# Kernel tuning notes

Hardware: AMD Instinct MI355X
Metric: run time of the kernel (lower is better)

The kernel has to match this reference:

```python
import jax, jax.numpy as jnp
import numpy as np

# hyper_params (mode='test')
PRE_NMS = 1000
POST_NMS = 300
IOU_TH = 0.7
VARIANCES = np.array([0.1, 0.1, 0.2, 0.2], dtype=np.float32)
FM = 64            # feature map height/width
ANCHOR_COUNT = 9   # 3 scales x 3 ratios


def _make_anchors():
    """Normalized [y1,x1,y2,x2] anchors on a FM x FM grid, 9 per cell."""
    scales = np.array([0.1, 0.2, 0.4], np.float32)
    ratios = np.array([0.5, 1.0, 2.0], np.float32)
    ws = (scales[:, None] * np.sqrt(ratios)[None, :]).reshape(-1)  # (9,)
    hs = (scales[:, None] / np.sqrt(ratios)[None, :]).reshape(-1)  # (9,)
    ctr = (np.arange(FM, dtype=np.float32) + 0.5) / FM
    cy, cx = np.meshgrid(ctr, ctr, indexing='ij')                  # (FM,FM)
    cy = cy[..., None]; cx = cx[..., None]                         # (FM,FM,1)
    anchors = np.stack([cy - 0.5 * hs, cx - 0.5 * ws,
                        cy + 0.5 * hs, cx + 0.5 * ws], axis=-1)    # (FM,FM,9,4)
    return jnp.asarray(anchors.reshape(-1, 4))                     # (36864,4)


def setup_inputs() -> dict:
    key = jax.random.key(0)
    k1, k2 = jax.random.split(key)
    B = 16
    rpn_bbox_deltas = jax.random.normal(k1, (B, FM, FM, ANCHOR_COUNT * 4), dtype=jnp.float32)
    rpn_labels = jax.random.uniform(k2, (B, FM, FM, ANCHOR_COUNT), dtype=jnp.float32)
    return {"rpn_bbox_deltas": rpn_bbox_deltas,
            "rpn_labels": rpn_labels,
            "anchors": _make_anchors()}


def _nms_single(boxes):
    """Greedy NMS on score-sorted boxes (N,4) -> (POST_NMS,4), zero-padded."""
    N = boxes.shape[0]
    y1, x1, y2, x2 = boxes[:, 0], boxes[:, 1], boxes[:, 2], boxes[:, 3]
    area = (y2 - y1) * (x2 - x1)                                   # (N,)
    iy1 = jnp.maximum(y1[:, None], y1[None, :])
    ix1 = jnp.maximum(x1[:, None], x1[None, :])
    iy2 = jnp.minimum(y2[:, None], y2[None, :])
    ix2 = jnp.minimum(x2[:, None], x2[None, :])
    inter = jnp.maximum(iy2 - iy1, 0.0) * jnp.maximum(ix2 - ix1, 0.0)
    iou = inter / jnp.maximum(area[:, None] + area[None, :] - inter, 1e-9)  # (N,N)
    idx = jnp.arange(N)

    def body(i, keep):
        # if box i survives, suppress later boxes with high overlap
        suppress = keep[i] & (iou[i] > IOU_TH) & (idx > i)
        return keep & ~suppress

    keep = jax.lax.fori_loop(0, N, body, jnp.ones((N,), dtype=bool))
    # stable sort: kept boxes first, original (score-descending) order preserved
    order = jnp.argsort(jnp.where(keep, 0, 1))[:POST_NMS]
    sel = boxes[order]
    valid = keep[order]
    # combined_non_max_suppression clips output boxes to [0,1] and zero-pads
    return jnp.where(valid[:, None], jnp.clip(sel, 0.0, 1.0), 0.0)


def reference(rpn_bbox_deltas, rpn_labels, anchors):
    B = rpn_bbox_deltas.shape[0]
    N = anchors.shape[0]
    deltas = rpn_bbox_deltas.reshape(B, N, 4) * jnp.asarray(VARIANCES)
    labels = rpn_labels.reshape(B, N)

    # decode deltas against anchors
    anc_h = anchors[:, 2] - anchors[:, 0]
    anc_w = anchors[:, 3] - anchors[:, 1]
    anc_cy = anchors[:, 0] + 0.5 * anc_h
    anc_cx = anchors[:, 1] + 0.5 * anc_w
    h = jnp.exp(deltas[..., 2]) * anc_h
    w = jnp.exp(deltas[..., 3]) * anc_w
    cy = deltas[..., 0] * anc_h + anc_cy
    cx = deltas[..., 1] * anc_w + anc_cx
    boxes = jnp.stack([cy - 0.5 * h, cx - 0.5 * w,
                       cy + 0.5 * h, cx + 0.5 * w], axis=-1)       # (B,N,4)

    # top-k by objectness score (descending, so NMS input is pre-sorted)
    _, pre_idx = jax.lax.top_k(labels, PRE_NMS)                    # (B,PRE_NMS)
    pre_boxes = jnp.take_along_axis(boxes, pre_idx[..., None], axis=1)  # (B,PRE_NMS,4)

    roi_bboxes = jax.vmap(_nms_single)(pre_boxes)                  # (B,POST_NMS,4)
    return jax.lax.stop_gradient(roi_bboxes)
```

## Files before the change

kernel.cpp:

```cpp
#include <hip/hip_runtime.h>
#include <stdint.h>

#pragma clang fp contract(off)

#define N_ANCH 36864
#define PRE_NMS 1000
#define POST_NMS 300
#define SEL_CAP 1024
#define NWAVE 16

#define SLICES 16
#define K1_NT 256
#define SLICE_KEYS 2304
#define KEYS_PT 9
#define SLICE_TOP 128
#define COMPACT_CAP 192
#define MERGE_CAP 2048

#define NCOPY 8
#define HSTR 257

#define M_WSTRIDE 1024
#define M_WORDS_PER_B 16384
#define WS_BOX_FLOATS_PER_B 5120

__device__ __forceinline__ uint32_t mono_key(float v) {
    uint32_t u = __float_as_uint(v);
    return (u & 0x80000000u) ? ~u : (u | 0x80000000u);
}

__device__ __forceinline__ float clip01(float x) {
    return fminf(fmaxf(x, 0.0f), 1.0f);
}

__device__ __forceinline__ uint64_t bcast64(uint64_t v, int srclane) {
    uint32_t lo = (uint32_t)v, hi = (uint32_t)(v >> 32);
    lo = __builtin_amdgcn_readlane(lo, srclane);
    hi = __builtin_amdgcn_readlane(hi, srclane);
    return ((uint64_t)hi << 32) | (uint64_t)lo;
}

__device__ __forceinline__ void scan256(const uint32_t* __restrict__ h, uint32_t K,
                                        uint32_t* shm, uint32_t& outBin, uint32_t& outKrem) {
    const int t    = threadIdx.x;
    const int lane = t & 63;
    const int wv   = t >> 6;
    const uint32_t q = h[t];
    uint32_t sfx = q, o;
    o = __shfl_down(sfx, 1);  if (lane < 63) sfx += o;
    o = __shfl_down(sfx, 2);  if (lane < 62) sfx += o;
    o = __shfl_down(sfx, 4);  if (lane < 60) sfx += o;
    o = __shfl_down(sfx, 8);  if (lane < 56) sfx += o;
    o = __shfl_down(sfx, 16); if (lane < 48) sfx += o;
    o = __shfl_down(sfx, 32); if (lane < 32) sfx += o;
    if (lane == 0) shm[wv] = sfx;
    __syncthreads();
    uint32_t wAbove = 0;
    for (int w2 = wv + 1; w2 < 4; ++w2) wAbove += shm[w2];
    const uint32_t above = wAbove + (sfx - q);
    if ((above < K) && (above + q >= K)) { shm[4] = (uint32_t)t; shm[5] = K - above; }
    __syncthreads();
    outBin  = shm[4];
    outKrem = shm[5];
}

__global__ __launch_bounds__(K1_NT) void k1s_slice_top(
    const float* __restrict__ labels,
    uint64_t* __restrict__ wsCand)
{
    const int s = blockIdx.x;
    const int b = blockIdx.y;
    const int t = threadIdx.x;
    const int lane = t & 63;

    __shared__ uint32_t hc[NCOPY * HSTR];
    __shared__ uint32_t red[256];
    __shared__ uint32_t shm[8];
    __shared__ uint64_t cand[COMPACT_CAP];
    __shared__ uint32_t scnt;

    const float* lab = labels + (size_t)b * N_ANCH + (size_t)s * SLICE_KEYS;
    uint32_t key[KEYS_PT];
#pragma unroll
    for (int r = 0; r < KEYS_PT; ++r)
        key[r] = mono_key(lab[r * K1_NT + t]);

    for (int i = t; i < NCOPY * HSTR; i += K1_NT) hc[i] = 0u;
    if (t == 0) scnt = 0u;
    __syncthreads();

    const int cbase = (lane & 7) * HSTR;
#pragma unroll
    for (int r = 0; r < KEYS_PT; ++r)
        atomicAdd(&hc[cbase + (key[r] >> 24)], 1u);
    __syncthreads();
    uint32_t sum = 0;
#pragma unroll
    for (int c = 0; c < NCOPY; ++c) sum += hc[c * HSTR + t];
    red[t] = sum;
    __syncthreads();
    uint32_t b0, krem;
    scan256(red, SLICE_TOP, shm, b0, krem);
    __syncthreads();

    red[t] = 0u;
    __syncthreads();
#pragma unroll
    for (int r = 0; r < KEYS_PT; ++r)
        if ((key[r] >> 24) == b0) atomicAdd(&red[(key[r] >> 16) & 0xFFu], 1u);
    __syncthreads();
    uint32_t b1, krem2;
    scan256(red, krem, shm, b1, krem2);
    const uint32_t thresh16 = (b0 << 8) | b1;

#pragma unroll
    for (int r = 0; r < KEYS_PT; ++r) {
        const uint32_t u = key[r];
        if ((u >> 16) >= thresh16) {
            const uint32_t gi = (uint32_t)(s * SLICE_KEYS + r * K1_NT + t);
            uint32_t pos = atomicAdd(&scnt, 1u);
            if (pos < COMPACT_CAP)
                cand[pos] = ((uint64_t)u << 32) | (uint64_t)(0xFFFFFFFFu - gi);
        }
    }
    __syncthreads();
    uint32_t c = scnt; if (c > COMPACT_CAP) c = COMPACT_CAP;
    if (t >= (int)c && t < COMPACT_CAP) cand[t] = 0ull;
    __syncthreads();

    if (t < COMPACT_CAP) {
        const uint64_t mine = cand[t];
        uint32_t rank = 0;
        for (int i = 0; i < COMPACT_CAP; i += 4)
            rank += (cand[i]     > mine) + (cand[i + 1] > mine)
                  + (cand[i + 2] > mine) + (cand[i + 3] > mine);
        if (t < (int)c && rank < SLICE_TOP)
            wsCand[((size_t)b * SLICES + s) * SLICE_TOP + rank] = mine;
    }
}

__global__ __launch_bounds__(K1_NT) void k1m_merge_decode(
    const float* __restrict__ deltas,
    const float* __restrict__ anchors,
    const uint64_t* __restrict__ wsCand,
    float* __restrict__ wsBox)
{
    const int chunk = blockIdx.x;
    const int b     = blockIdx.y;
    const int t     = threadIdx.x;

    __shared__ uint64_t keyA[MERGE_CAP];
    const uint64_t* c2 = wsCand + (size_t)b * MERGE_CAP;
    for (int i = t; i < MERGE_CAP; i += K1_NT) keyA[i] = c2[i];
    __syncthreads();

    if (t < SLICE_TOP) {
        const uint64_t mine = keyA[chunk * SLICE_TOP + t];
        uint32_t rank = 0;
#pragma unroll
        for (int r = 0; r < SLICES; ++r) {
            const uint64_t* a = &keyA[r * SLICE_TOP];
            uint32_t lo = 0;
#pragma unroll
            for (uint32_t s2 = 128; s2 > 0; s2 >>= 1)
                if (lo + s2 <= 128u && a[lo + s2 - 1] > mine) lo += s2;
            rank += lo;
        }
        if (rank < PRE_NMS) {
            uint32_t idx = 0xFFFFFFFFu - (uint32_t)(mine & 0xFFFFFFFFull);
            float4 d4 = *(const float4*)(deltas + ((size_t)b * N_ANCH + idx) * 4);
            float4 a4 = *(const float4*)(anchors + (size_t)idx * 4);
            float anc_h  = a4.z - a4.x;
            float anc_w  = a4.w - a4.y;
            float anc_cy = a4.x + 0.5f * anc_h;
            float anc_cx = a4.y + 0.5f * anc_w;
            float dy = d4.x * 0.1f, dx = d4.y * 0.1f;
            float dh = d4.z * 0.2f, dw = d4.w * 0.2f;
            float h  = expf(dh) * anc_h;
            float w  = expf(dw) * anc_w;
            float cy = dy * anc_h + anc_cy;
            float cx = dx * anc_w + anc_cx;
            float y1 = cy - 0.5f * h, x1 = cx - 0.5f * w;
            float y2 = cy + 0.5f * h, x2 = cx + 0.5f * w;
            float* wb = wsBox + (size_t)b * WS_BOX_FLOATS_PER_B;
            wb[rank]              = y1;
            wb[SEL_CAP + rank]    = x1;
            wb[2*SEL_CAP + rank]  = y2;
            wb[3*SEL_CAP + rank]  = x2;
            wb[4*SEL_CAP + rank]  = (y2 - y1) * (x2 - x1);
        }
    }
}

__global__ __launch_bounds__(1024) void k2_iou_matrix(
    const float* __restrict__ wsBox,
    uint64_t* __restrict__ wsM)
{
    const int gx   = blockIdx.x;
    const int b    = blockIdx.y;
    const int t    = threadIdx.x;
    const int lane = t & 63;
    const int wave = t >> 6;

    int cb, r0, r1;
    if (gx < 16) { cb = gx;     r0 = 0;   r1 = 64 * (cb + 1); if (r1 > 512) r1 = 512; }
    else         { cb = gx - 8; r0 = 512; r1 = 64 * (cb + 1); }
    if (r1 > PRE_NMS) r1 = PRE_NMS;

    __shared__ float s[5 * SEL_CAP];
    const float4* b4 = (const float4*)(wsBox + (size_t)b * WS_BOX_FLOATS_PER_B);
    float4* s4 = (float4*)s;
    for (int i = t; i < (5 * SEL_CAP) / 4; i += 1024) s4[i] = b4[i];
    __syncthreads();

    float* ly1 = s;
    float* lx1 = s + SEL_CAP;
    float* ly2 = s + 2 * SEL_CAP;
    float* lx2 = s + 3 * SEL_CAP;
    float* lar = s + 4 * SEL_CAP;

    const int j = cb * 64 + lane;
    const float y1j = ly1[j], x1j = lx1[j], y2j = ly2[j], x2j = lx2[j], aj = lar[j];

    uint64_t* Mb = wsM + (size_t)b * M_WORDS_PER_B + (size_t)cb * M_WSTRIDE;
    for (int i = r0 + wave; i < r1; i += NWAVE) {
        float iy1 = fmaxf(ly1[i], y1j);
        float ix1 = fmaxf(lx1[i], x1j);
        float iy2 = fminf(ly2[i], y2j);
        float ix2 = fminf(lx2[i], x2j);
        float ih = iy2 - iy1; if (ih < 0.f) ih = 0.f;
        float iw = ix2 - ix1; if (iw < 0.f) iw = 0.f;
        float inter = ih * iw;
        float denom = lar[i] + aj - inter;
        if (denom < 1e-9f) denom = 1e-9f;
        float iou = inter / denom;
        bool sup = (j > i) && (iou > 0.7f);
        uint64_t mask = __ballot(sup ? 1 : 0);
        if (lane == 0) Mb[i] = mask;
    }
}

__global__ __launch_bounds__(1024) void k3_reduce_out(
    const float* __restrict__ wsBox,
    const uint64_t* __restrict__ wsM,
    float* __restrict__ out)
{
    const int b    = blockIdx.x;
    const int t    = threadIdx.x;
    const int lane = t & 63;
    const int wave = t >> 6;

    __shared__ uint64_t remv[16];
    __shared__ uint64_t keepW[16];
    __shared__ uint32_t wordPref[16];

    const uint64_t* Mg = wsM + (size_t)b * M_WORDS_PER_B;

    if (t < 16) remv[t] = 0ull;
    __syncthreads();

    for (int w = 0; w < 16; ++w) {
        if (wave == 0) {
            const uint64_t m = Mg[(size_t)w * M_WSTRIDE + 64 * w + lane];
            uint64_t cur = remv[w];
            if (w < 15) {
#pragma unroll
                for (int bp = 0; bp < 64; ++bp) {
                    const uint64_t mb = bcast64(m, bp);
                    cur |= ((cur >> bp) & 1ull) ? 0ull : mb;
                }
            } else {
#pragma unroll
                for (int bp = 0; bp < 40; ++bp) {
                    const uint64_t mb = bcast64(m, bp);
                    cur |= ((cur >> bp) & 1ull) ? 0ull : mb;
                }
            }
            const uint64_t valid = (w == 15) ? ((1ull << 40) - 1ull) : ~0ull;
            if (lane == 0) keepW[w] = (~cur) & valid;
        }
        __syncthreads();
        if (wave > w) {
            const uint64_t km = keepW[w];
            uint64_t v = Mg[(size_t)wave * M_WSTRIDE + 64 * w + lane];
            v = ((km >> lane) & 1ull) ? v : 0ull;
            v |= __shfl_xor(v, 32);
            v |= __shfl_xor(v, 16);
            v |= __shfl_xor(v, 8);
            v |= __shfl_xor(v, 4);
            v |= __shfl_xor(v, 2);
            v |= __shfl_xor(v, 1);
            if (lane == 0) remv[wave] |= v;
        }
        __syncthreads();
    }

    if (t == 0) {
        uint32_t acc = 0u;
        for (int w = 0; w < 16; ++w) {
            wordPref[w] = acc;
            acc += (uint32_t)__popcll(keepW[w]);
        }
    }
    float* ob = out + (size_t)b * (POST_NMS * 4);
    for (int i = t; i < POST_NMS * 4; i += 1024) ob[i] = 0.0f;
    __syncthreads();

    if (t < PRE_NMS) {
        const int w = t >> 6, bpos = t & 63;
        uint64_t kw = keepW[w];
        if ((kw >> bpos) & 1ull) {
            uint32_t rank = wordPref[w] +
                            (uint32_t)__popcll(kw & ((1ull << bpos) - 1ull));
            if (rank < POST_NMS) {
                const float* wb = wsBox + (size_t)b * WS_BOX_FLOATS_PER_B;
                float* o = ob + (size_t)rank * 4;
                o[0] = clip01(wb[t]);
                o[1] = clip01(wb[SEL_CAP + t]);
                o[2] = clip01(wb[2*SEL_CAP + t]);
                o[3] = clip01(wb[3*SEL_CAP + t]);
            }
        }
    }
}

extern "C" void kernel_launch(void* const* d_in, const int* in_sizes, int n_in,
                              void* d_out, int out_size, void* d_ws, size_t ws_size,
                              hipStream_t stream) {
    const float* deltas  = (const float*)d_in[0];
    const float* labels  = (const float*)d_in[1];
    const float* anchors = (const float*)d_in[2];
    float* out = (float*)d_out;
    const int B = in_sizes[1] / N_ANCH;

    char* p = (char*)d_ws;
    uint64_t* wsCand = (uint64_t*)p;
    float*    wsBox  = (float*)(p + (size_t)B * MERGE_CAP * 8);
    uint64_t* wsM    = (uint64_t*)(p + (size_t)B * MERGE_CAP * 8
                                     + (size_t)B * WS_BOX_FLOATS_PER_B * 4);

    k1s_slice_top<<<dim3(SLICES, B), K1_NT, 0, stream>>>(labels, wsCand);
    k1m_merge_decode<<<dim3(SLICES, B), K1_NT, 0, stream>>>(deltas, anchors, wsCand, wsBox);
    k2_iou_matrix<<<dim3(24, B), 1024, 0, stream>>>(wsBox, wsM);
    k3_reduce_out<<<B, 1024, 0, stream>>>(wsBox, wsM, out);
}
```

Measured before the change: 131.5 us.

## Pipeline NMS suppression-mask reduction across waves with prefetched diagonal blocks

The serial greedy NMS reduction in k3_reduce_out now drops one of its two barriers per word. Wave 0 prefetches the next diagonal and superdiagonal mask words and applies the superdiagonal suppression to the next word itself. The other waves apply suppression from the previous word's keep mask one iteration late, so their work overlaps wave 0's serial scan. The intent is to shorten the critical path of the 16-step loop, at the cost of more complex lagged bookkeeping, which risks correctness if the skew is handled wrongly.

Measured after the change: 122.6 us. 6.7% less time.

```diff
diff --git a/kernel.cpp b/kernel.cpp
--- a/kernel.cpp
+++ b/kernel.cpp
@@ -257,12 +257,24 @@
     const uint64_t* Mg = wsM + (size_t)b * M_WORDS_PER_B;
 
     if (t < 16) remv[t] = 0ull;
+
+    uint64_t mDiag = 0ull, mSup = 0ull, selfC = 0ull;
+    if (wave == 0) {
+        mDiag = Mg[lane];
+        mSup  = Mg[(size_t)1 * M_WSTRIDE + lane];
+    }
     __syncthreads();
 
     for (int w = 0; w < 16; ++w) {
         if (wave == 0) {
-            const uint64_t m = Mg[(size_t)w * M_WSTRIDE + 64 * w + lane];
-            uint64_t cur = remv[w];
+            const uint64_t m  = mDiag;
+            const uint64_t ms = mSup;
+            if (w < 15) {
+                mDiag = Mg[(size_t)(w + 1) * M_WSTRIDE + 64 * (w + 1) + lane];
+                if (w < 14)
+                    mSup = Mg[(size_t)(w + 2) * M_WSTRIDE + 64 * (w + 1) + lane];
+            }
+            uint64_t cur = remv[w] | selfC;
             if (w < 15) {
 #pragma unroll
                 for (int bp = 0; bp < 64; ++bp) {
@@ -277,12 +289,21 @@
                 }
             }
             const uint64_t valid = (w == 15) ? ((1ull << 40) - 1ull) : ~0ull;
-            if (lane == 0) keepW[w] = (~cur) & valid;
-        }
-        __syncthreads();
-        if (wave > w) {
-            const uint64_t km = keepW[w];
-            uint64_t v = Mg[(size_t)wave * M_WSTRIDE + 64 * w + lane];
+            const uint64_t keep = (~cur) & valid;
+            if (lane == 0) keepW[w] = keep;
+            if (w < 15) {
+                uint64_t v = ((keep >> lane) & 1ull) ? ms : 0ull;
+                v |= __shfl_xor(v, 32);
+                v |= __shfl_xor(v, 16);
+                v |= __shfl_xor(v, 8);
+                v |= __shfl_xor(v, 4);
+                v |= __shfl_xor(v, 2);
+                v |= __shfl_xor(v, 1);
+                selfC = v;
+            }
+        } else if (w >= 1 && wave > w) {
+            const uint64_t km = keepW[w - 1];
+            uint64_t v = Mg[(size_t)wave * M_WSTRIDE + 64 * (w - 1) + lane];
             v = ((km >> lane) & 1ull) ? v : 0ull;
             v |= __shfl_xor(v, 32);
             v |= __shfl_xor(v, 16);
```
